# Kernel optimization log

Measured on AMD Instinct MI355X. Metric: run time of the kernel, lower is better.

Reference implementation:

```python
import jax, jax.numpy as jnp
import numpy as np

N_QUBITS = 6
N_LAYERS = 2
DIM = 2 ** N_QUBITS  # 64


def _apply_1q(state, U, q):
    """Apply a 1-qubit gate U on qubit q. state: (B, 2,...,2); U: (2,2) or (B,2,2)."""
    s = jnp.moveaxis(state, 1 + q, -1)
    if U.ndim == 3:  # batched gate (angle embedding)
        s = jnp.einsum('bij,b...j->b...i', U, s)
    else:
        s = jnp.einsum('ij,...j->...i', U, s)
    return jnp.moveaxis(s, -1, 1 + q)


def _cnot(state, c, t):
    """CNOT with control qubit c, target qubit t on (B, 2,...,2) state."""
    ax_c = 1 + c
    s0 = jax.lax.index_in_dim(state, 0, ax_c, keepdims=False)
    s1 = jax.lax.index_in_dim(state, 1, ax_c, keepdims=False)
    ax_t = 1 + t if t < c else t  # target axis index after removing control axis
    s1 = jnp.flip(s1, axis=ax_t)  # X on target where control=1
    return jnp.stack([s0, s1], axis=ax_c)


def _rot(phi, theta, omega):
    """PennyLane Rot(phi,theta,omega) = RZ(omega) RY(theta) RZ(phi), as a (2,2) complex matrix."""
    ct = jnp.cos(theta / 2)
    st = jnp.sin(theta / 2)
    ep = jnp.exp(-0.5j * (phi + omega))
    em = jnp.exp(0.5j * (phi - omega))
    row0 = jnp.stack([ep * ct, -em * st])
    row1 = jnp.stack([jnp.conj(em) * st, jnp.conj(ep) * ct])
    return jnp.stack([row0, row1]).astype(jnp.complex64)


def _circuit(angles, weights):
    """AngleEmbedding (RX) + StronglyEntanglingLayers + per-qubit <Z>. angles: (B, 6)."""
    B = angles.shape[0]
    state = jnp.zeros((B,) + (2,) * N_QUBITS, jnp.complex64)
    state = state.at[(slice(None),) + (0,) * N_QUBITS].set(1.0)

    # AngleEmbedding: RX(angle_q) on each qubit (batched gates)
    for q in range(N_QUBITS):
        half = angles[:, q] / 2
        ct = jnp.cos(half).astype(jnp.complex64)
        st = jnp.sin(half)
        U = jnp.stack([jnp.stack([ct, -1j * st], -1),
                       jnp.stack([-1j * st, ct], -1)], -2)  # (B,2,2)
        state = _apply_1q(state, U, q)

    # StronglyEntanglingLayers: per-layer Rot on each qubit, then CNOT ring with range r
    for l in range(N_LAYERS):
        for q in range(N_QUBITS):
            state = _apply_1q(state, _rot(weights[l, q, 0], weights[l, q, 1], weights[l, q, 2]), q)
        r = (l % (N_QUBITS - 1)) + 1
        for q in range(N_QUBITS):
            state = _cnot(state, q, (q + r) % N_QUBITS)

    probs = (state.real ** 2 + state.imag ** 2).reshape(B, DIM)  # (B, 64)
    # <Z_q> = sum_i probs[i] * (1 - 2*bit_q(i)); qubit 0 is the most-significant axis
    bits = (jnp.arange(DIM)[None, :] >> (N_QUBITS - 1 - jnp.arange(N_QUBITS))[:, None]) & 1
    signs = (1 - 2 * bits).astype(probs.dtype)  # (6, 64)
    return probs @ signs.T  # (B, 6)


def setup_inputs() -> dict:
    key = jax.random.key(0)
    k1, k2, k3, k4 = jax.random.split(key, 4)
    B, D = 65536, 512
    x = jax.random.normal(k1, (B, D), jnp.float32)
    W = jax.random.normal(k2, (N_QUBITS, D), jnp.float32) / np.float32(np.sqrt(D))
    b = jax.random.normal(k3, (N_QUBITS,), jnp.float32) * 0.01
    weights = jax.random.uniform(k4, (N_LAYERS, N_QUBITS, 3), jnp.float32, 0.0, 2 * np.pi)
    return {"x": x, "W": W, "b": b, "weights": weights}


def reference(x, W, b, weights):
    z = x @ W.T + b                                   # (B, 6)
    z = z / jnp.linalg.norm(z, axis=1, keepdims=True)  # L2 normalize per row
    return _circuit(z, weights)                        # (B, 6) Pauli-Z expvals
```

## Files before the change

kernel.cpp:

```cpp
#include <hip/hip_runtime.h>
#include <math.h>

#define NQ 6
#define NLAYERS 2
#define ROW_D 512

typedef short short8 __attribute__((ext_vector_type(8)));
typedef float f32x4 __attribute__((ext_vector_type(4)));

__device__ __forceinline__ ushort f2bf(float f) {
    unsigned u = __float_as_uint(f);
    return (ushort)((u + 0x7fffu + ((u >> 16) & 1u)) >> 16);
}
__device__ __forceinline__ float bf2f(ushort h) {
    return __uint_as_float((unsigned)h << 16);
}
__device__ __forceinline__ unsigned cvt2bf(float lo, float hi) {
    unsigned r;
    asm("v_cvt_pk_bf16_f32 %0, %1, %2" : "=v"(r) : "v"(lo), "v"(hi));
    return r;
}
__device__ __forceinline__ float merge_red(float u, float v, int m, int lane) {
    float send = (lane & m) ? u : v;
    float recv = __shfl_xor(send, m, 64);
    return ((lane & m) ? v : u) + recv;
}

__global__ __launch_bounds__(256) void gen_tables(
    const float* __restrict__ weights, const float* __restrict__ W,
    ushort* __restrict__ ws)
{
    const int tid = threadIdx.x;
    {
        const int base = (blockIdx.x * 256 + tid) * 2;
        #pragma unroll
        for (int e = 0; e < 2; ++e) {
            const int i = base + e;
            const int n = i >> 9, k = i & 511;
            const int w = k >> 5, g = (k >> 3) & 3, e2 = k & 7;
            const int ksrc = w * 32 + ((e2 < 4) ? (4 * g + e2) : (16 + 4 * g + e2 - 4));
            ushort v = 0;
            if (n < NQ) {
                v = f2bf(W[(n << 9) | ksrc]);
            } else if (n >= 8 && n < 8 + NQ) {
                const float wv = W[((n - 8) << 9) | ksrc];
                v = f2bf(wv - bf2f(f2bf(wv)));
            }
            ws[8192 + i] = v;
        }
    }

    __shared__ __align__(16) float gmat[NLAYERS * NQ * 8];
    if (tid < NLAYERS * NQ) {
        float phi = weights[tid * 3 + 0];
        float th  = weights[tid * 3 + 1];
        float om  = weights[tid * 3 + 2];
        float st, ct, sA, cA, sB, cB;
        __sincosf(0.5f * th, &st, &ct);
        __sincosf(0.5f * (phi + om), &sA, &cA);
        __sincosf(0.5f * (phi - om), &sB, &cB);
        float* g = &gmat[tid * 8];
        g[0] =  cA * ct;  g[1] = -sA * ct;
        g[2] = -cB * st;  g[3] = -sB * st;
        g[4] =  cA * ct;  g[5] =  sA * ct;
        g[6] =  cB * st;  g[7] = -sB * st;
    }
    __syncthreads();

    const int lane = tid & 63;
    const int wave = tid >> 6;
    const int jj = blockIdx.x * 4 + wave;

    int srcA = lane;
    #pragma unroll
    for (int q = NQ - 1; q >= 0; --q) {
        const int t = (q + 1) % NQ;
        srcA ^= ((srcA >> (5 - q)) & 1) << (5 - t);
    }
    int srcB = lane;
    #pragma unroll
    for (int q = NQ - 1; q >= 0; --q) {
        const int t = (q + 2) % NQ;
        srcB ^= ((srcB >> (5 - q)) & 1) << (5 - t);
    }
    const int adA = srcA << 2, adB = srcB << 2;

    float sr = (lane == jj) ? 1.f : 0.f;
    float si = 0.f;
    #pragma unroll
    for (int l = 0; l < NLAYERS; ++l) {
        #pragma unroll
        for (int q = 0; q < NQ; ++q) {
            const int bp = 5 - q, m = 1 << bp;
            const int bit = (lane >> bp) & 1;
            const float4 g = *reinterpret_cast<const float4*>(
                &gmat[((l * NQ + q) << 3) + (bit << 2)]);
            float pr = __shfl_xor(sr, m, 64);
            float pi = __shfl_xor(si, m, 64);
            float nr = g.x * sr - g.y * si + g.z * pr - g.w * pi;
            float ni = g.x * si + g.y * sr + g.z * pi + g.w * pr;
            sr = nr; si = ni;
        }
        const int ad = (l == 0) ? adA : adB;
        sr = __int_as_float(__builtin_amdgcn_ds_bpermute(ad, __float_as_int(sr)));
        si = __int_as_float(__builtin_amdgcn_ds_bpermute(ad, __float_as_int(si)));
    }

    const int pc = __popc(jj) & 3;
    float r2, i2;
    if      (pc == 1) { r2 =  si; i2 = -sr; }
    else if (pc == 2) { r2 = -sr; i2 = -si; }
    else if (pc == 3) { r2 = -si; i2 =  sr; }
    else              { r2 =  sr; i2 =  si; }
    ws[lane * 64 + jj]        = f2bf(r2);
    ws[4096 + lane * 64 + jj] = f2bf(i2);
}

__global__ __launch_bounds__(256, 4) void qmain(
    const float* __restrict__ x, const float* __restrict__ bvec,
    const ushort* __restrict__ ws, float* __restrict__ out, int B)
{
    __shared__ short8 Mlds[2][64][8];
    __shared__ short8 Wlds[16][64];
    __shared__ float2 trans[4][144];
    const int tid = threadIdx.x;

    const short8* mg = reinterpret_cast<const short8*>(ws);
    #pragma unroll
    for (int i = 0; i < 4; ++i) {
        const int idx = tid + i * 256;
        short8 v = mg[idx];
        const int mat = idx >> 9, row = (idx >> 3) & 63, c = idx & 7;
        Mlds[mat][row][c ^ (row & 7)] = v;
    }
    #pragma unroll
    for (int i = 0; i < 4; ++i) {
        const int idx = tid + i * 256;
        short8 v = mg[1024 + idx];
        const int n = idx >> 6, c = idx & 63;
        Wlds[n][c ^ (n & 7)] = v;
    }
    __syncthreads();

    const int lane = tid & 63;
    const int wave = tid >> 6;
    const int g  = lane >> 4;
    const int l4 = lane & 15;
    const int swz = l4 & 7;
    const int rowbase = blockIdx.x * 64 + wave * 16;

    f32x4 zacc = {0.f, 0.f, 0.f, 0.f};
    const float* xrow = x + (size_t)(rowbase + l4) * ROW_D + g * 4;
    #pragma unroll 8
    for (int kt = 0; kt < 16; ++kt) {
        const float4 xa = *reinterpret_cast<const float4*>(xrow + kt * 32);
        const float4 xb = *reinterpret_cast<const float4*>(xrow + kt * 32 + 16);
        uint4 u;
        u.x = cvt2bf(xa.x, xa.y);
        u.y = cvt2bf(xa.z, xa.w);
        u.z = cvt2bf(xb.x, xb.y);
        u.w = cvt2bf(xb.z, xb.w);
        const short8 af = __builtin_bit_cast(short8, u);
        const short8 bw = Wlds[l4][(kt * 4 + g) ^ swz];
        zacc = __builtin_amdgcn_mfma_f32_16x16x32_bf16(af, bw, zacc, 0, 0, 0);
    }

    const float bn = (l4 < NQ) ? bvec[l4] : 0.f;
    #pragma unroll
    for (int reg = 0; reg < 4; ++reg) {
        const float zlo = __shfl_xor(zacc[reg], 8, 64);
        const float zv = zacc[reg] + zlo + bn;
        float s2 = (l4 < NQ) ? zv * zv : 0.f;
        s2 += __shfl_xor(s2, 1, 64);
        s2 += __shfl_xor(s2, 2, 64);
        s2 += __shfl_xor(s2, 4, 64);
        s2 += __shfl_xor(s2, 8, 64);
        const float ang = 0.5f * zv * rsqrtf(s2);
        float sv, cv;
        __sincosf(ang, &sv, &cv);
        if (l4 < NQ)
            trans[wave][(g * 4 + reg) * 9 + l4] = make_float2(cv, sv);
    }

    float cq[NQ], sq[NQ];
    #pragma unroll
    for (int q = 0; q < NQ; ++q) {
        const float2 cs = trans[wave][l4 * 9 + q];
        cq[q] = cs.x; sq[q] = cs.y;
    }
    float m45[4];
    m45[0] = cq[4] * cq[5]; m45[1] = cq[4] * sq[5];
    m45[2] = sq[4] * cq[5]; m45[3] = sq[4] * sq[5];
    float pl[8];
    #pragma unroll
    for (int j = 0; j < 8; ++j)
        pl[j] = ((j & 4) ? sq[3] : cq[3]) * m45[j & 3];
    const float t12 = ((g & 2) ? sq[1] : cq[1]) * ((g & 1) ? sq[2] : cq[2]);
    const float ph0 = cq[0] * t12;
    const float ph1 = sq[0] * t12;
    uint4 ua, ub;
    ua.x = cvt2bf(ph0 * pl[0], ph0 * pl[1]);
    ua.y = cvt2bf(ph0 * pl[2], ph0 * pl[3]);
    ua.z = cvt2bf(ph0 * pl[4], ph0 * pl[5]);
    ua.w = cvt2bf(ph0 * pl[6], ph0 * pl[7]);
    ub.x = cvt2bf(ph1 * pl[0], ph1 * pl[1]);
    ub.y = cvt2bf(ph1 * pl[2], ph1 * pl[3]);
    ub.z = cvt2bf(ph1 * pl[4], ph1 * pl[5]);
    ub.w = cvt2bf(ph1 * pl[6], ph1 * pl[7]);
    const short8 a0 = __builtin_bit_cast(short8, ua);
    const short8 a1 = __builtin_bit_cast(short8, ub);

    f32x4 cre[4] = {}, cim[4] = {};
    #pragma unroll
    for (int nt = 0; nt < 4; ++nt) {
        const int brow = nt * 16 + l4;
        const short8 br0 = Mlds[0][brow][(g)     ^ swz];
        const short8 br1 = Mlds[0][brow][(4 + g) ^ swz];
        const short8 bi0 = Mlds[1][brow][(g)     ^ swz];
        const short8 bi1 = Mlds[1][brow][(4 + g) ^ swz];
        cre[nt] = __builtin_amdgcn_mfma_f32_16x16x32_bf16(a0, br0, cre[nt], 0, 0, 0);
        cre[nt] = __builtin_amdgcn_mfma_f32_16x16x32_bf16(a1, br1, cre[nt], 0, 0, 0);
        cim[nt] = __builtin_amdgcn_mfma_f32_16x16x32_bf16(a0, bi0, cim[nt], 0, 0, 0);
        cim[nt] = __builtin_amdgcn_mfma_f32_16x16x32_bf16(a1, bi1, cim[nt], 0, 0, 0);
    }

    const int col = l4;
    #pragma unroll
    for (int reg = 0; reg < 4; ++reg) {
        const float p0 = cre[0][reg] * cre[0][reg] + cim[0][reg] * cim[0][reg];
        const float p1 = cre[1][reg] * cre[1][reg] + cim[1][reg] * cim[1][reg];
        const float p2 = cre[2][reg] * cre[2][reg] + cim[2][reg] * cim[2][reg];
        const float p3 = cre[3][reg] * cre[3][reg] + cim[3][reg] * cim[3][reg];
        float t  = (p0 + p1) + (p2 + p3);
        float y0 = (p0 + p1) - (p2 + p3);
        float y1 = (p0 + p2) - (p1 + p3);
        #pragma unroll
        for (int m = 1; m <= 8; m <<= 1) {
            float rcv = __shfl_xor(t, m, 64);
            t = (lane & m) ? (rcv - t) : (t + rcv);
        }
        float y = merge_red(y0, y1, 1, lane);
        y += __shfl_xor(y, 2, 64);
        y += __shfl_xor(y, 4, 64);
        y += __shfl_xor(y, 8, 64);
        const size_t orow = (size_t)(rowbase + g * 4 + reg) * 6;
        if      (col == 0) { out[orow + 0] = y; }
        else if (col == 1) { out[orow + 1] = y; out[orow + 5] = t; }
        else if (col == 2) { out[orow + 4] = t; }
        else if (col == 4) { out[orow + 3] = t; }
        else if (col == 8) { out[orow + 2] = t; }
    }
}

extern "C" void kernel_launch(void* const* d_in, const int* in_sizes, int n_in,
                              void* d_out, int out_size, void* d_ws, size_t ws_size,
                              hipStream_t stream) {
    const float* x  = (const float*)d_in[0];
    const float* W  = (const float*)d_in[1];
    const float* bv = (const float*)d_in[2];
    const float* wt = (const float*)d_in[3];
    float* out = (float*)d_out;
    ushort* ws = (ushort*)d_ws;
    const int B = in_sizes[0] / ROW_D;
    gen_tables<<<16, 256, 0, stream>>>(wt, W, ws);
    qmain<<<B / 64, 256, 0, stream>>>(x, bv, ws, out, B);
}
```

Measured before the change: 34.33 us.

## Stage x tiles into LDS via global_load_lds and read circuit matrix from global

Replaces the per-lane float4 global loads of x with direct global-to-LDS 16-byte async loads into a swizzled 64x64 float tile, staged per 64-column chunk with barriers between chunks. The W table layout is simplified to natural k order to match the new LDS read pattern. The circuit matrix is now read straight from global/L2 instead of being copied into LDS, freeing LDS for the x tile. The intent is better coalescing and less VGPR pressure on the x stream, at the cost of 16 barriers per block and no double buffering, so load latency is exposed at every stage.

```diff
diff --git a/kernel.cpp b/kernel.cpp
--- a/kernel.cpp
+++ b/kernel.cpp
@@ -24,6 +24,11 @@
     float send = (lane & m) ? u : v;
     float recv = __shfl_xor(send, m, 64);
     return ((lane & m) ? v : u) + recv;
+}
+__device__ __forceinline__ void gload16(const float* g, void* ldsbase) {
+    __builtin_amdgcn_global_load_lds(
+        (const __attribute__((address_space(1))) void*)g,
+        (__attribute__((address_space(3))) void*)ldsbase, 16, 0, 0);
 }
 
 __global__ __launch_bounds__(256) void gen_tables(
@@ -37,14 +42,12 @@
         for (int e = 0; e < 2; ++e) {
             const int i = base + e;
             const int n = i >> 9, k = i & 511;
-            const int w = k >> 5, g = (k >> 3) & 3, e2 = k & 7;
-            const int ksrc = w * 32 + ((e2 < 4) ? (4 * g + e2) : (16 + 4 * g + e2 - 4));
             ushort v = 0;
             if (n < NQ) {
-                v = f2bf(W[(n << 9) | ksrc]);
+                v = f2bf(W[(n << 9) | k]);
             } else if (n >= 8 && n < 8 + NQ) {
-                const float wv = W[((n - 8) << 9) | ksrc];
-                v = f2bf(wv - bf2f(f2bf(wv)));
+                const float w = W[((n - 8) << 9) | k];
+                v = f2bf(w - bf2f(f2bf(w)));
             }
             ws[8192 + i] = v;
         }
@@ -120,19 +123,12 @@
     const float* __restrict__ x, const float* __restrict__ bvec,
     const ushort* __restrict__ ws, float* __restrict__ out, int B)
 {
-    __shared__ short8 Mlds[2][64][8];
+    __shared__ float xt[64][64];
     __shared__ short8 Wlds[16][64];
     __shared__ float2 trans[4][144];
     const int tid = threadIdx.x;
 
     const short8* mg = reinterpret_cast<const short8*>(ws);
-    #pragma unroll
-    for (int i = 0; i < 4; ++i) {
-        const int idx = tid + i * 256;
-        short8 v = mg[idx];
-        const int mat = idx >> 9, row = (idx >> 3) & 63, c = idx & 7;
-        Mlds[mat][row][c ^ (row & 7)] = v;
-    }
     #pragma unroll
     for (int i = 0; i < 4; ++i) {
         const int idx = tid + i * 256;
@@ -140,7 +136,6 @@
         const int n = idx >> 6, c = idx & 63;
         Wlds[n][c ^ (n & 7)] = v;
     }
-    __syncthreads();
 
     const int lane = tid & 63;
     const int wave = tid >> 6;
@@ -148,22 +143,51 @@
     const int l4 = lane & 15;
     const int swz = l4 & 7;
     const int rowbase = blockIdx.x * 64 + wave * 16;
+    const int blkbase = blockIdx.x * 64;
+
+    const int srow_l = lane >> 4;
+    const int csb = lane & 15;
+
+    #define STAGE(p)                                                          \
+        _Pragma("unroll")                                                     \
+        for (int k = 0; k < 4; ++k) {                                         \
+            const int row = wave * 16 + k * 4 + srow_l;                       \
+            const int c = csb ^ (row & 7);                                    \
+            const float* gp = x + (size_t)(blkbase + row) * ROW_D             \
+                              + (p) * 64 + c * 4;                             \
+            gload16(gp, &xt[wave * 16 + k * 4][0]);                           \
+        }
+
+    STAGE(0)
 
     f32x4 zacc = {0.f, 0.f, 0.f, 0.f};
-    const float* xrow = x + (size_t)(rowbase + l4) * ROW_D + g * 4;
-    #pragma unroll 8
-    for (int kt = 0; kt < 16; ++kt) {
-        const float4 xa = *reinterpret_cast<const float4*>(xrow + kt * 32);
-        const float4 xb = *reinterpret_cast<const float4*>(xrow + kt * 32 + 16);
-        uint4 u;
-        u.x = cvt2bf(xa.x, xa.y);
-        u.y = cvt2bf(xa.z, xa.w);
-        u.z = cvt2bf(xb.x, xb.y);
-        u.w = cvt2bf(xb.z, xb.w);
-        const short8 af = __builtin_bit_cast(short8, u);
-        const short8 bw = Wlds[l4][(kt * 4 + g) ^ swz];
-        zacc = __builtin_amdgcn_mfma_f32_16x16x32_bf16(af, bw, zacc, 0, 0, 0);
-    }
+    const float* xtr = &xt[wave * 16 + l4][0];
+    #pragma unroll
+    for (int p = 0; p < 8; ++p) {
+        __syncthreads();
+        #pragma unroll
+        for (int kt2 = 0; kt2 < 2; ++kt2) {
+            const int kt = p * 2 + kt2;
+            const int cbase = kt2 * 8 + 2 * g;
+            const float4 fa = *reinterpret_cast<const float4*>(
+                xtr + ((cbase ^ swz) << 2));
+            const float4 fb = *reinterpret_cast<const float4*>(
+                xtr + (((cbase + 1) ^ swz) << 2));
+            uint4 u;
+            u.x = cvt2bf(fa.x, fa.y);
+            u.y = cvt2bf(fa.z, fa.w);
+            u.z = cvt2bf(fb.x, fb.y);
+            u.w = cvt2bf(fb.z, fb.w);
+            const short8 af = __builtin_bit_cast(short8, u);
+            const short8 bw = Wlds[l4][(kt * 4 + g) ^ swz];
+            zacc = __builtin_amdgcn_mfma_f32_16x16x32_bf16(af, bw, zacc, 0, 0, 0);
+        }
+        if (p < 7) {
+            __syncthreads();
+            STAGE(p + 1)
+        }
+    }
+    #undef STAGE
 
     const float bn = (l4 < NQ) ? bvec[l4] : 0.f;
     #pragma unroll
@@ -214,10 +238,10 @@
     #pragma unroll
     for (int nt = 0; nt < 4; ++nt) {
         const int brow = nt * 16 + l4;
-        const short8 br0 = Mlds[0][brow][(g)     ^ swz];
-        const short8 br1 = Mlds[0][brow][(4 + g) ^ swz];
-        const short8 bi0 = Mlds[1][brow][(g)     ^ swz];
-        const short8 bi1 = Mlds[1][brow][(4 + g) ^ swz];
+        const short8 br0 = mg[brow * 8 + g];
+        const short8 br1 = mg[brow * 8 + 4 + g];
+        const short8 bi0 = mg[512 + brow * 8 + g];
+        const short8 bi1 = mg[512 + brow * 8 + 4 + g];
         cre[nt] = __builtin_amdgcn_mfma_f32_16x16x32_bf16(a0, br0, cre[nt], 0, 0, 0);
         cre[nt] = __builtin_amdgcn_mfma_f32_16x16x32_bf16(a1, br1, cre[nt], 0, 0, 0);
         cim[nt] = __builtin_amdgcn_mfma_f32_16x16x32_bf16(a0, bi0, cim[nt], 0, 0, 0);
```

Result: slower. 39.50 us (+15.0%).

## Convert W to bf16 hi/lo in qmain and read circuit matrix from global

Applied to the files above, without the earlier changes.

The W-to-bf16 hi/lo split conversion moves out of gen_tables and into each qmain block, which now reads fp32 W directly when it fills its LDS tile. The 64x64 circuit unitary is no longer staged in LDS; MFMA B-operands are loaded straight from global/L2. This cuts LDS usage and a staging pass per block, and it shortens gen_tables. In exchange every block repeats the W conversion and issues global loads for the unitary just before its MFMAs.

```diff
diff --git a/kernel.cpp b/kernel.cpp
--- a/kernel.cpp
+++ b/kernel.cpp
@@ -27,29 +27,9 @@
 }
 
 __global__ __launch_bounds__(256) void gen_tables(
-    const float* __restrict__ weights, const float* __restrict__ W,
-    ushort* __restrict__ ws)
+    const float* __restrict__ weights, ushort* __restrict__ ws)
 {
     const int tid = threadIdx.x;
-    {
-        const int base = (blockIdx.x * 256 + tid) * 2;
-        #pragma unroll
-        for (int e = 0; e < 2; ++e) {
-            const int i = base + e;
-            const int n = i >> 9, k = i & 511;
-            const int w = k >> 5, g = (k >> 3) & 3, e2 = k & 7;
-            const int ksrc = w * 32 + ((e2 < 4) ? (4 * g + e2) : (16 + 4 * g + e2 - 4));
-            ushort v = 0;
-            if (n < NQ) {
-                v = f2bf(W[(n << 9) | ksrc]);
-            } else if (n >= 8 && n < 8 + NQ) {
-                const float wv = W[((n - 8) << 9) | ksrc];
-                v = f2bf(wv - bf2f(f2bf(wv)));
-            }
-            ws[8192 + i] = v;
-        }
-    }
-
     __shared__ __align__(16) float gmat[NLAYERS * NQ * 8];
     if (tid < NLAYERS * NQ) {
         float phi = weights[tid * 3 + 0];
@@ -117,27 +97,32 @@
 }
 
 __global__ __launch_bounds__(256, 4) void qmain(
-    const float* __restrict__ x, const float* __restrict__ bvec,
-    const ushort* __restrict__ ws, float* __restrict__ out, int B)
+    const float* __restrict__ x, const float* __restrict__ W,
+    const float* __restrict__ bvec, const ushort* __restrict__ ws,
+    float* __restrict__ out, int B)
 {
-    __shared__ short8 Mlds[2][64][8];
     __shared__ short8 Wlds[16][64];
     __shared__ float2 trans[4][144];
     const int tid = threadIdx.x;
 
-    const short8* mg = reinterpret_cast<const short8*>(ws);
     #pragma unroll
     for (int i = 0; i < 4; ++i) {
         const int idx = tid + i * 256;
-        short8 v = mg[idx];
-        const int mat = idx >> 9, row = (idx >> 3) & 63, c = idx & 7;
-        Mlds[mat][row][c ^ (row & 7)] = v;
-    }
-    #pragma unroll
-    for (int i = 0; i < 4; ++i) {
-        const int idx = tid + i * 256;
-        short8 v = mg[1024 + idx];
         const int n = idx >> 6, c = idx & 63;
+        const int ktc = c >> 2, gg = c & 3;
+        short8 v = {0, 0, 0, 0, 0, 0, 0, 0};
+        const int nsrc = (n < 8) ? n : (n - 8);
+        if (nsrc < NQ) {
+            const float* wsrc = W + (nsrc << 9) + ktc * 32 + 4 * gg;
+            const float4 wa = *reinterpret_cast<const float4*>(wsrc);
+            const float4 wb = *reinterpret_cast<const float4*>(wsrc + 16);
+            float e[8] = {wa.x, wa.y, wa.z, wa.w, wb.x, wb.y, wb.z, wb.w};
+            #pragma unroll
+            for (int j = 0; j < 8; ++j) {
+                const ushort hi = f2bf(e[j]);
+                v[j] = (n < 8) ? (short)hi : (short)f2bf(e[j] - bf2f(hi));
+            }
+        }
         Wlds[n][c ^ (n & 7)] = v;
     }
     __syncthreads();
@@ -148,6 +133,7 @@
     const int l4 = lane & 15;
     const int swz = l4 & 7;
     const int rowbase = blockIdx.x * 64 + wave * 16;
+    const short8* mg = reinterpret_cast<const short8*>(ws);
 
     f32x4 zacc = {0.f, 0.f, 0.f, 0.f};
     const float* xrow = x + (size_t)(rowbase + l4) * ROW_D + g * 4;
@@ -214,10 +200,10 @@
     #pragma unroll
     for (int nt = 0; nt < 4; ++nt) {
         const int brow = nt * 16 + l4;
-        const short8 br0 = Mlds[0][brow][(g)     ^ swz];
-        const short8 br1 = Mlds[0][brow][(4 + g) ^ swz];
-        const short8 bi0 = Mlds[1][brow][(g)     ^ swz];
-        const short8 bi1 = Mlds[1][brow][(4 + g) ^ swz];
+        const short8 br0 = mg[brow * 8 + g];
+        const short8 br1 = mg[brow * 8 + 4 + g];
+        const short8 bi0 = mg[512 + brow * 8 + g];
+        const short8 bi1 = mg[512 + brow * 8 + 4 + g];
         cre[nt] = __builtin_amdgcn_mfma_f32_16x16x32_bf16(a0, br0, cre[nt], 0, 0, 0);
         cre[nt] = __builtin_amdgcn_mfma_f32_16x16x32_bf16(a1, br1, cre[nt], 0, 0, 0);
         cim[nt] = __builtin_amdgcn_mfma_f32_16x16x32_bf16(a0, bi0, cim[nt], 0, 0, 0);
@@ -262,6 +248,6 @@
     float* out = (float*)d_out;
     ushort* ws = (ushort*)d_ws;
     const int B = in_sizes[0] / ROW_D;
-    gen_tables<<<16, 256, 0, stream>>>(wt, W, ws);
-    qmain<<<B / 64, 256, 0, stream>>>(x, bv, ws, out, B);
-}
+    gen_tables<<<16, 256, 0, stream>>>(wt, ws);
+    qmain<<<B / 64, 256, 0, stream>>>(x, W, bv, ws, out, B);
+}
```

Result: slower. 40.62 us (+18.3%).
